# Performance work log

Hardware: AMD Instinct MI355X
Metric: run time of the kernel (lower is better)

Reference implementation:

```python
import jax, jax.numpy as jnp
import numpy as np

NUM_EMBEDDINGS = 1024
EMBEDDING_DIM = 256
COMMITMENT_COST = 0.25
N_TOKENS = 65536


def setup_inputs() -> dict:
    key = jax.random.key(0)
    k1, k2 = jax.random.split(key)
    z = jax.random.normal(k1, (N_TOKENS, EMBEDDING_DIM), dtype=jnp.float32)
    # codebook init as in the module: uniform in [-1/K, 1/K]
    embedding = jax.random.uniform(
        k2, (NUM_EMBEDDINGS, EMBEDDING_DIM),
        minval=-1.0 / NUM_EMBEDDINGS, maxval=1.0 / NUM_EMBEDDINGS,
        dtype=jnp.float32)
    return {"z": z, "embedding": embedding}


def reference(z, embedding):
    # squared euclidean distances: ||z||^2 + ||e||^2 - 2 z.e^T   -> [N, K]
    z_sq = jnp.sum(z ** 2, axis=1, keepdims=True)          # [N, 1]
    emb_sq = jnp.sum(embedding ** 2, axis=1)               # [K]
    dot = jnp.dot(z, embedding.T)                          # [N, K]
    distances = z_sq + emb_sq - 2.0 * dot
    indices = jnp.argmin(distances, axis=1)                # [N]
    z_q = embedding[indices]                               # [N, D] gather
    loss = (jnp.mean((jax.lax.stop_gradient(z) - z_q) ** 2)
            + COMMITMENT_COST * jnp.mean((jax.lax.stop_gradient(z_q) - z) ** 2))
    z_q_st = z + jax.lax.stop_gradient(z_q - z)            # straight-through
    return (z_q_st, loss, indices)
```

## Files before the change

kernel.cpp:

```cpp
#include <hip/hip_runtime.h>
#include <hip/hip_bf16.h>

#define NTOK   65536
#define KCODES 1024
#define DIM    256
#define LOSS_OFF ((size_t)NTOK * DIM)
#define IDX_OFF  (LOSS_OFF + 1)

#define MARGA 2e-4f

#define SC_ZSQ    0
#define SC_A1     65536
#define SC_LOSS2  131072
#define SC_ESQ    196608
#define SC_ESQNH  197632
#define SC_PART   198656
#define SC_WCNT   198720
#define SC_WCNT2  198721
#define SC_CNTG   198784
#define SC_LISTS  264320
#define SC_WLIST  788608
#define SC_WLIST2 854144
#define SC_EHIMG  858240
#define SC_ZIMG   989312
#define SC_PAIRD  9377920

typedef __attribute__((ext_vector_type(8))) short short8;
typedef __attribute__((ext_vector_type(4))) float f32x4;

__device__ __forceinline__ unsigned f2bf(float x) {
    unsigned u = __float_as_uint(x);
    return (u + 0x7FFFu + ((u >> 16) & 1u)) >> 16;
}

__device__ __forceinline__ void gload16(const void* g, void* l) {
    __builtin_amdgcn_global_load_lds((const __attribute__((address_space(1))) unsigned int*)g,
                                     (__attribute__((address_space(3))) unsigned int*)l,
                                     16, 0, 0);
}

__device__ __forceinline__ float faithful_d(const float* __restrict__ z,
                                            const float* __restrict__ emb,
                                            float zsq, float esq, int tok, int c) {
    const float4* zr = (const float4*)(z + (size_t)tok * DIM);
    const float4* er = (const float4*)(emb + (size_t)c * DIM);
    float acc = 0.f;
#pragma unroll 8
    for (int q = 0; q < 64; ++q) {
        float4 a = zr[q], b = er[q];
        acc = fmaf(a.x, b.x, acc); acc = fmaf(a.y, b.y, acc);
        acc = fmaf(a.z, b.z, acc); acc = fmaf(a.w, b.w, acc);
    }
    float t1 = zsq + esq;
    return t1 - 2.0f * acc;
}

__device__ __forceinline__ float np_rowsq256_wave(const float* row, int sub) {
    const int j = sub & 7, half = sub >> 3;
    const float* a = row + half * 128 + j;
    float r = 0.f;
#pragma unroll
    for (int i = 0; i < 16; ++i) {
        float v = a[i * 8];
        float sq = v * v;
        asm volatile("" : "+v"(sq));
        r += sq;
    }
    float t = r + __shfl_xor(r, 1, 64);
    t = t + __shfl_xor(t, 2, 64);
    t = t + __shfl_xor(t, 4, 64);
    t = t + __shfl_xor(t, 8, 64);
    return t;
}

__global__ __launch_bounds__(256) void vq_prep_esq(const float* __restrict__ emb,
                                                   float* __restrict__ esq,
                                                   float* __restrict__ esqnh,
                                                   int* __restrict__ wcnt,
                                                   int* __restrict__ wcnt2) {
    if (blockIdx.x == 0 && threadIdx.x == 0) { *wcnt = 0; *wcnt2 = 0; }
    int code = blockIdx.x * 16 + (threadIdx.x >> 4);
    int sub = threadIdx.x & 15;
    float tot = np_rowsq256_wave(emb + (size_t)code * DIM, sub);
    if (sub == 0) { esq[code] = tot; esqnh[code] = -0.5f * tot; }
}

__global__ __launch_bounds__(256) void vq_prep_z(const float* __restrict__ z,
                                                 float* __restrict__ zsq,
                                                 unsigned short* __restrict__ zimg) {
    int tok = blockIdx.x * 16 + (threadIdx.x >> 4);
    int sub = threadIdx.x & 15;
    float tot = np_rowsq256_wave(z + (size_t)tok * DIM, sub);
    if (sub == 0) zsq[tok] = tot;

    const float* src = z + (size_t)tok * DIM + sub * 16;
    float4 v0 = *(const float4*)&src[0],  v1 = *(const float4*)&src[4];
    float4 v2 = *(const float4*)&src[8],  v3 = *(const float4*)&src[12];
    uint4 p0, p1;
    p0.x = f2bf(v0.x) | (f2bf(v0.y) << 16);  p0.y = f2bf(v0.z) | (f2bf(v0.w) << 16);
    p0.z = f2bf(v1.x) | (f2bf(v1.y) << 16);  p0.w = f2bf(v1.z) | (f2bf(v1.w) << 16);
    p1.x = f2bf(v2.x) | (f2bf(v2.y) << 16);  p1.y = f2bf(v2.z) | (f2bf(v2.w) << 16);
    p1.z = f2bf(v3.x) | (f2bf(v3.y) << 16);  p1.w = f2bf(v3.z) | (f2bf(v3.w) << 16);

    int bid = tok >> 6, tf = (tok >> 4) & 3, sl = tok & 15;
    int g0 = sub * 2, g1 = g0 + 1;
    size_t rowbase = ((size_t)bid * 4 + tf) * 8;
    char* d0 = (char*)zimg + ((rowbase + (g0 >> 2)) << 10) + (((g0 & 3) * 16 + sl) << 4);
    char* d1 = (char*)zimg + ((rowbase + (g1 >> 2)) << 10) + (((g1 & 3) * 16 + sl) << 4);
    *(uint4*)d0 = p0;
    *(uint4*)d1 = p1;
}

__global__ __launch_bounds__(256) void vq_prep_eimg(const float* __restrict__ emb,
                                                    unsigned short* __restrict__ img) {
    int job = blockIdx.x * 256 + threadIdx.x;
    int code = job >> 3, ks = job & 7;
    int cc = (code >> 6) & 3, lcl = (code >> 8) * 64 + (code & 63);
    const float* src = emb + (size_t)code * DIM + ks * 32;
    char* base = (char*)img + (size_t)(cc * 8 + ks) * 16384;
#pragma unroll
    for (int q = 0; q < 4; ++q) {
        float4 v0 = *(const float4*)&src[q * 8];
        float4 v1 = *(const float4*)&src[q * 8 + 4];
        uint4 p;
        p.x = f2bf(v0.x) | (f2bf(v0.y) << 16);
        p.y = f2bf(v0.z) | (f2bf(v0.w) << 16);
        p.z = f2bf(v1.x) | (f2bf(v1.y) << 16);
        p.w = f2bf(v1.z) | (f2bf(v1.w) << 16);
        *(uint4*)(base + lcl * 64 + ((q * 16) ^ (((lcl >> 1) & 3) << 4))) = p;
    }
}

template<int PASS>
__global__ __launch_bounds__(256, 2) void vq_gemm(const unsigned short* __restrict__ zimg,
                                                  const unsigned short* __restrict__ img,
                                                  const float* __restrict__ esqnh,
                                                  const float* __restrict__ zsq,
                                                  float* __restrict__ a1,
                                                  int* __restrict__ wcnt,
                                                  int* __restrict__ wlist,
                                                  int* __restrict__ cntg,
                                                  int* __restrict__ listsg,
                                                  float* __restrict__ loss2,
                                                  float* __restrict__ dout) {
    __shared__ __align__(16) short eh_s[2][8192];
    __shared__ float a1w_s[4][64];
    __shared__ int cnt_s[64];
    __shared__ int lists_s[512];

    const int tid = threadIdx.x, bid = blockIdx.x;
    const int w = tid >> 6, l = tid & 63;
    const int t0 = bid * 64;

    short8 zf[4][8];
#pragma unroll
    for (int tf = 0; tf < 4; ++tf)
#pragma unroll
        for (int ks = 0; ks < 8; ++ks)
            zf[tf][ks] = *(const short8*)((const char*)zimg +
                           ((((size_t)bid * 4 + tf) * 8 + ks) << 10) + (size_t)l * 16);

    if (PASS == 2 && tid < 64) cnt_s[tid] = 0;
    {
        const char* gs = (const char*)img + w * 4096 + (size_t)l * 16;
        char* ld = (char*)&eh_s[0][0] + w * 4096;
#pragma unroll
        for (int i = 0; i < 4; ++i) gload16(gs + i * 1024, ld + i * 1024);
    }
    __syncthreads();

    float thrv[4], amax[4];
#pragma unroll
    for (int tf = 0; tf < 4; ++tf) {
        amax[tf] = -3.4e38f;
        if (PASS == 2) thrv[tf] = a1[t0 + tf * 16 + (l & 15)] - MARGA;
    }

    f32x4 acc[4][4];

#pragma unroll
    for (int c = 0; c < 4; ++c) {
#pragma unroll
        for (int f = 0; f < 4; ++f) {
            f32x4 e4 = *(const f32x4*)&esqnh[w * 256 + c * 64 + f * 16 + (l >> 4) * 4];
#pragma unroll
            for (int tf = 0; tf < 4; ++tf) acc[f][tf] = e4;
        }
#pragma unroll
        for (int ks = 0; ks < 8; ++ks) {
            int s = c * 8 + ks, buf = s & 1;
            if (s < 31) {
                const char* gs = (const char*)img + (size_t)(s + 1) * 16384 + w * 4096 + (size_t)l * 16;
                char* ld = (char*)&eh_s[buf ^ 1][0] + w * 4096;
#pragma unroll
                for (int i = 0; i < 4; ++i) gload16(gs + i * 1024, ld + i * 1024);
            }
            short8 afr[4];
#pragma unroll
            for (int f = 0; f < 4; ++f) {
                int lcl = w * 64 + f * 16 + (l & 15);
                int byte = lcl * 64 + (((l >> 4) * 16) ^ (((lcl >> 1) & 3) << 4));
                afr[f] = *(const short8*)((const char*)&eh_s[buf][0] + byte);
            }
#pragma unroll
            for (int f = 0; f < 4; ++f)
#pragma unroll
                for (int tf = 0; tf < 4; ++tf)
                    acc[f][tf] = __builtin_amdgcn_mfma_f32_16x16x32_bf16(
                        afr[f], zf[tf][ks], acc[f][tf], 0, 0, 0);
            __syncthreads();
        }
        if (PASS == 1) {
#pragma unroll
            for (int tf = 0; tf < 4; ++tf) {
                float m0 = fmaxf(fmaxf(acc[0][tf][0], acc[0][tf][1]), fmaxf(acc[0][tf][2], acc[0][tf][3]));
                float m1 = fmaxf(fmaxf(acc[1][tf][0], acc[1][tf][1]), fmaxf(acc[1][tf][2], acc[1][tf][3]));
                float m2 = fmaxf(fmaxf(acc[2][tf][0], acc[2][tf][1]), fmaxf(acc[2][tf][2], acc[2][tf][3]));
                float m3 = fmaxf(fmaxf(acc[3][tf][0], acc[3][tf][1]), fmaxf(acc[3][tf][2], acc[3][tf][3]));
                amax[tf] = fmaxf(amax[tf], fmaxf(fmaxf(m0, m1), fmaxf(m2, m3)));
            }
        } else {
#pragma unroll
            for (int tf = 0; tf < 4; ++tf) {
                int tokl = tf * 16 + (l & 15);
#pragma unroll
                for (int f = 0; f < 4; ++f)
#pragma unroll
                    for (int r = 0; r < 4; ++r) {
                        float a = acc[f][tf][r];
                        if (a >= thrv[tf]) {
                            int code = w * 256 + c * 64 + f * 16 + (l >> 4) * 4 + r;
                            int pos = atomicAdd(&cnt_s[tokl], 1);
                            if (pos < 8) lists_s[tokl * 8 + pos] = code;
                        }
                    }
            }
        }
    }

    if (PASS == 1) {
#pragma unroll
        for (int tf = 0; tf < 4; ++tf) {
            float m = amax[tf];
            m = fmaxf(m, __shfl_xor(m, 16, 64));
            m = fmaxf(m, __shfl_xor(m, 32, 64));
            if (l < 16) a1w_s[w][tf * 16 + l] = m;
        }
        __syncthreads();
        if (tid < 64)
            a1[t0 + tid] = fmaxf(fmaxf(a1w_s[0][tid], a1w_s[1][tid]),
                                 fmaxf(a1w_s[2][tid], a1w_s[3][tid]));
    } else {
        __syncthreads();
        if (tid < 64) {
            int t = t0 + tid, ct = cnt_s[tid];
            if (ct == 1) {
                dout[IDX_OFF + t] = (float)lists_s[tid * 8];
                loss2[t] = fmaf(-2.f, a1[t], zsq[t]);
            } else {
                int pos = atomicAdd(wcnt, 1);
                wlist[pos] = t;
                cntg[t] = ct;
                int m = ct < 8 ? ct : 8;
                for (int i = 0; i < m; ++i) listsg[t * 8 + i] = lists_s[tid * 8 + i];
            }
        }
    }
}

__global__ __launch_bounds__(256) void vq_pairs(const float* __restrict__ z,
                                                const float* __restrict__ emb,
                                                const float* __restrict__ zsq,
                                                const float* __restrict__ esq,
                                                const int* __restrict__ wcnt,
                                                const int* __restrict__ wlist,
                                                const int* __restrict__ cntg,
                                                const int* __restrict__ listsg,
                                                int* __restrict__ wcnt2,
                                                int* __restrict__ wlist2,
                                                float* __restrict__ paird) {
    const int n = wcnt[0];
    const int total = 8 * n;
    for (int p = blockIdx.x * 256 + threadIdx.x; p < total; p += 2048 * 256) {
        int q = p >> 3, slot = p & 7;
        int tok = wlist[q];
        int ct = cntg[tok];
        if (ct == 0 || ct > 8) {
            if (slot == 0) {
                int pos = atomicAdd(wcnt2, 1);
                if (pos < 4096) wlist2[pos] = tok;
            }
            continue;
        }
        if (slot >= ct) continue;
        int code = listsg[tok * 8 + slot];
        paird[p] = faithful_d(z, emb, zsq[tok], esq[code], tok, code);
    }
}

__global__ __launch_bounds__(256) void vq_pick(const float* __restrict__ paird,
                                               const int* __restrict__ wcnt,
                                               const int* __restrict__ wlist,
                                               const int* __restrict__ cntg,
                                               const int* __restrict__ listsg,
                                               float* __restrict__ loss2,
                                               float* __restrict__ dout) {
    const int n = wcnt[0];
    for (int q = blockIdx.x * 256 + threadIdx.x; q < n; q += 256 * 256) {
        int tok = wlist[q];
        int ct = cntg[tok];
        if (ct == 0 || ct > 8) continue;
        float db = paird[q * 8];
        int cb = listsg[tok * 8];
        for (int i = 1; i < ct; ++i) {
            float d = paird[q * 8 + i];
            int c = listsg[tok * 8 + i];
            if (d < db || (d == db && c < cb)) { db = d; cb = c; }
        }
        dout[IDX_OFF + tok] = (float)cb;
        loss2[tok] = db;
    }
}

__global__ __launch_bounds__(256) void vq_decide_scan(const float* __restrict__ z,
                                                      const float* __restrict__ emb,
                                                      const float* __restrict__ zsq,
                                                      const float* __restrict__ esq,
                                                      const int* __restrict__ wcnt2,
                                                      const int* __restrict__ wlist2,
                                                      float* __restrict__ loss2,
                                                      float* __restrict__ dout) {
    __shared__ __align__(16) float zrow[DIM];
    __shared__ float dred[256];
    __shared__ int   ired[256];
    int n = wcnt2[0];
    if (n > 4096) n = 4096;
    const int tid = threadIdx.x;
    for (int job = blockIdx.x; job < n; job += 128) {
        int tok = wlist2[job];
        __syncthreads();
        if (tid < 64) ((float4*)zrow)[tid] = ((const float4*)(z + (size_t)tok * DIM))[tid];
        __syncthreads();
        float zq = zsq[tok];
        float a0 = 0.f, a1v = 0.f, a2 = 0.f, a3 = 0.f;
        const float4* e0 = (const float4*)(emb + (size_t)(tid      ) * DIM);
        const float4* e1 = (const float4*)(emb + (size_t)(tid + 256) * DIM);
        const float4* e2 = (const float4*)(emb + (size_t)(tid + 512) * DIM);
        const float4* e3 = (const float4*)(emb + (size_t)(tid + 768) * DIM);
#pragma unroll
        for (int seg = 0; seg < 4; ++seg) {
#pragma unroll
            for (int qq = 0; qq < 16; ++qq) {
                float4 a = ((float4*)zrow)[seg * 16 + qq];
                float4 b0 = e0[seg * 16 + qq], b1 = e1[seg * 16 + qq];
                float4 b2 = e2[seg * 16 + qq], b3 = e3[seg * 16 + qq];
                a0 = fmaf(a.x, b0.x, a0); a0 = fmaf(a.y, b0.y, a0);
                a0 = fmaf(a.z, b0.z, a0); a0 = fmaf(a.w, b0.w, a0);
                a1v = fmaf(a.x, b1.x, a1v); a1v = fmaf(a.y, b1.y, a1v);
                a1v = fmaf(a.z, b1.z, a1v); a1v = fmaf(a.w, b1.w, a1v);
                a2 = fmaf(a.x, b2.x, a2); a2 = fmaf(a.y, b2.y, a2);
                a2 = fmaf(a.z, b2.z, a2); a2 = fmaf(a.w, b2.w, a2);
                a3 = fmaf(a.x, b3.x, a3); a3 = fmaf(a.y, b3.y, a3);
                a3 = fmaf(a.z, b3.z, a3); a3 = fmaf(a.w, b3.w, a3);
            }
        }
        float d0 = (zq + esq[tid      ]) - 2.0f * a0;
        float d1 = (zq + esq[tid + 256]) - 2.0f * a1v;
        float d2 = (zq + esq[tid + 512]) - 2.0f * a2;
        float d3 = (zq + esq[tid + 768]) - 2.0f * a3;
        float db = d0; int cb = tid;
        if (d1 < db) { db = d1; cb = tid + 256; }
        if (d2 < db) { db = d2; cb = tid + 512; }
        if (d3 < db) { db = d3; cb = tid + 768; }
        dred[tid] = db; ired[tid] = cb;
        __syncthreads();
        for (int step = 128; step >= 1; step >>= 1) {
            if (tid < step) {
                float od = dred[tid + step]; int oi = ired[tid + step];
                if (od < dred[tid] || (od == dred[tid] && oi < ired[tid])) {
                    dred[tid] = od; ired[tid] = oi;
                }
            }
            __syncthreads();
        }
        if (tid == 0) {
            dout[IDX_OFF + tok] = (float)ired[0];
            loss2[tok] = dred[0];
        }
    }
}

__global__ __launch_bounds__(256) void vq_sum(const float* __restrict__ loss2,
                                              float* __restrict__ part) {
    __shared__ float ws[4];
    float s = 0.f;
#pragma unroll
    for (int q = 0; q < 4; ++q)
        s += loss2[blockIdx.x * 1024 + q * 256 + threadIdx.x];
#pragma unroll
    for (int m = 1; m < 64; m <<= 1) s += __shfl_xor(s, m, 64);
    if ((threadIdx.x & 63) == 0) ws[threadIdx.x >> 6] = s;
    __syncthreads();
    if (threadIdx.x == 0) part[blockIdx.x] = ws[0] + ws[1] + ws[2] + ws[3];
}

__global__ __launch_bounds__(64) void vq_final(const float* __restrict__ part,
                                               float* __restrict__ dout) {
    double s = (double)part[threadIdx.x];
#pragma unroll
    for (int m = 1; m < 64; m <<= 1) s += __shfl_xor(s, m, 64);
    if (threadIdx.x == 0) dout[LOSS_OFF] = (float)(s * 1.25 / 16777216.0);
}

__global__ __launch_bounds__(256) void vq_gather(const float* __restrict__ emb,
                                                 float* __restrict__ dout) {
    const int w = threadIdx.x >> 6, l = threadIdx.x & 63;
    for (int tok = blockIdx.x * 4 + w; tok < NTOK; tok += 2048 * 4) {
        int widx = (int)dout[IDX_OFF + tok];
        float4 ev = *(const float4*)&emb[(size_t)widx * DIM + l * 4];
        *(float4*)&dout[(size_t)tok * DIM + l * 4] = ev;
    }
}

extern "C" void kernel_launch(void* const* d_in, const int* in_sizes, int n_in,
                              void* d_out, int out_size, void* d_ws, size_t ws_size,
                              hipStream_t stream) {
    const float* z   = (const float*)d_in[0];
    const float* emb = (const float*)d_in[1];
    float* out = (float*)d_out;

    float* zsq   = out + SC_ZSQ;
    float* a1    = out + SC_A1;
    float* loss2 = out + SC_LOSS2;
    float* esq   = out + SC_ESQ;
    float* esqnh = out + SC_ESQNH;
    float* part  = out + SC_PART;
    int*   wcnt  = (int*)(out + SC_WCNT);
    int*   wcnt2 = (int*)(out + SC_WCNT2);
    int*   cntg  = (int*)(out + SC_CNTG);
    int*   listsg= (int*)(out + SC_LISTS);
    int*   wlist = (int*)(out + SC_WLIST);
    int*   wlist2= (int*)(out + SC_WLIST2);
    float* paird = out + SC_PAIRD;
    unsigned short* img  = (unsigned short*)(out + SC_EHIMG);
    unsigned short* zimg = (unsigned short*)(out + SC_ZIMG);

    vq_prep_esq <<<64,   256, 0, stream>>>(emb, esq, esqnh, wcnt, wcnt2);
    vq_prep_z   <<<4096, 256, 0, stream>>>(z, zsq, zimg);
    vq_prep_eimg<<<32,   256, 0, stream>>>(emb, img);
    vq_gemm<1>  <<<1024, 256, 0, stream>>>(zimg, img, esqnh, zsq, a1, wcnt, wlist, cntg, listsg, loss2, out);
    vq_gemm<2>  <<<1024, 256, 0, stream>>>(zimg, img, esqnh, zsq, a1, wcnt, wlist, cntg, listsg, loss2, out);
    vq_pairs    <<<2048, 256, 0, stream>>>(z, emb, zsq, esq, wcnt, wlist, cntg, listsg, wcnt2, wlist2, paird);
    vq_pick     <<<256,  256, 0, stream>>>(paird, wcnt, wlist, cntg, listsg, loss2, out);
    vq_decide_scan<<<128, 256, 0, stream>>>(z, emb, zsq, esq, wcnt2, wlist2, loss2, out);
    vq_sum      <<<64,   256, 0, stream>>>(loss2, part);
    vq_final    <<<1,    64,  0, stream>>>(part, out);
    vq_gather   <<<2048, 256, 0, stream>>>(emb, out);
}
```

Before: 160.1 us.

## Fuse two-pass GEMM argmin into a single pass with running-max candidate filtering

The separate max pass and candidate-collection pass of the bf16 MFMA distance GEMM are merged into one kernel. Each chunk tracks a running per-token max, records candidates above the running threshold together with their scores in shared memory, then re-filters them against the final max. This halves the GEMM work and the reads of z and the codebook. In exchange, early chunks can admit more candidates, which risks overflowing the 16-slot buffer and pushing more tokens to the slow fallback path.

```diff
diff --git a/kernel.cpp b/kernel.cpp
--- a/kernel.cpp
+++ b/kernel.cpp
@@ -10,7 +10,6 @@
 #define MARGA 2e-4f
 
 #define SC_ZSQ    0
-#define SC_A1     65536
 #define SC_LOSS2  131072
 #define SC_ESQ    196608
 #define SC_ESQNH  197632
@@ -131,12 +130,10 @@
     }
 }
 
-template<int PASS>
 __global__ __launch_bounds__(256, 2) void vq_gemm(const unsigned short* __restrict__ zimg,
                                                   const unsigned short* __restrict__ img,
                                                   const float* __restrict__ esqnh,
                                                   const float* __restrict__ zsq,
-                                                  float* __restrict__ a1,
                                                   int* __restrict__ wcnt,
                                                   int* __restrict__ wlist,
                                                   int* __restrict__ cntg,
@@ -145,8 +142,9 @@
                                                   float* __restrict__ dout) {
     __shared__ __align__(16) short eh_s[2][8192];
     __shared__ float a1w_s[4][64];
-    __shared__ int cnt_s[64];
-    __shared__ int lists_s[512];
+    __shared__ int   cnt_s[64];
+    __shared__ int   lists_s[64 * 16];
+    __shared__ float avals_s[64 * 16];
 
     const int tid = threadIdx.x, bid = blockIdx.x;
     const int w = tid >> 6, l = tid & 63;
@@ -160,7 +158,7 @@
             zf[tf][ks] = *(const short8*)((const char*)zimg +
                            ((((size_t)bid * 4 + tf) * 8 + ks) << 10) + (size_t)l * 16);
 
-    if (PASS == 2 && tid < 64) cnt_s[tid] = 0;
+    if (tid < 64) cnt_s[tid] = 0;
     {
         const char* gs = (const char*)img + w * 4096 + (size_t)l * 16;
         char* ld = (char*)&eh_s[0][0] + w * 4096;
@@ -169,13 +167,7 @@
     }
     __syncthreads();
 
-    float thrv[4], amax[4];
-#pragma unroll
-    for (int tf = 0; tf < 4; ++tf) {
-        amax[tf] = -3.4e38f;
-        if (PASS == 2) thrv[tf] = a1[t0 + tf * 16 + (l & 15)] - MARGA;
-    }
-
+    float m_run[4] = {-3.4e38f, -3.4e38f, -3.4e38f, -3.4e38f};
     f32x4 acc[4][4];
 
 #pragma unroll
@@ -210,59 +202,68 @@
                         afr[f], zf[tf][ks], acc[f][tf], 0, 0, 0);
             __syncthreads();
         }
-        if (PASS == 1) {
-#pragma unroll
-            for (int tf = 0; tf < 4; ++tf) {
-                float m0 = fmaxf(fmaxf(acc[0][tf][0], acc[0][tf][1]), fmaxf(acc[0][tf][2], acc[0][tf][3]));
-                float m1 = fmaxf(fmaxf(acc[1][tf][0], acc[1][tf][1]), fmaxf(acc[1][tf][2], acc[1][tf][3]));
-                float m2 = fmaxf(fmaxf(acc[2][tf][0], acc[2][tf][1]), fmaxf(acc[2][tf][2], acc[2][tf][3]));
-                float m3 = fmaxf(fmaxf(acc[3][tf][0], acc[3][tf][1]), fmaxf(acc[3][tf][2], acc[3][tf][3]));
-                amax[tf] = fmaxf(amax[tf], fmaxf(fmaxf(m0, m1), fmaxf(m2, m3)));
-            }
-        } else {
-#pragma unroll
-            for (int tf = 0; tf < 4; ++tf) {
-                int tokl = tf * 16 + (l & 15);
-#pragma unroll
-                for (int f = 0; f < 4; ++f)
-#pragma unroll
-                    for (int r = 0; r < 4; ++r) {
-                        float a = acc[f][tf][r];
-                        if (a >= thrv[tf]) {
-                            int code = w * 256 + c * 64 + f * 16 + (l >> 4) * 4 + r;
-                            int pos = atomicAdd(&cnt_s[tokl], 1);
-                            if (pos < 8) lists_s[tokl * 8 + pos] = code;
+#pragma unroll
+        for (int tf = 0; tf < 4; ++tf) {
+            float m0 = fmaxf(fmaxf(acc[0][tf][0], acc[0][tf][1]), fmaxf(acc[0][tf][2], acc[0][tf][3]));
+            float m1 = fmaxf(fmaxf(acc[1][tf][0], acc[1][tf][1]), fmaxf(acc[1][tf][2], acc[1][tf][3]));
+            float m2 = fmaxf(fmaxf(acc[2][tf][0], acc[2][tf][1]), fmaxf(acc[2][tf][2], acc[2][tf][3]));
+            float m3 = fmaxf(fmaxf(acc[3][tf][0], acc[3][tf][1]), fmaxf(acc[3][tf][2], acc[3][tf][3]));
+            float tm = fmaxf(fmaxf(m0, m1), fmaxf(m2, m3));
+            tm = fmaxf(tm, __shfl_xor(tm, 16, 64));
+            tm = fmaxf(tm, __shfl_xor(tm, 32, 64));
+            m_run[tf] = fmaxf(m_run[tf], tm);
+            float thr = m_run[tf] - MARGA;
+            int tokl = tf * 16 + (l & 15);
+#pragma unroll
+            for (int f = 0; f < 4; ++f)
+#pragma unroll
+                for (int r = 0; r < 4; ++r) {
+                    float a = acc[f][tf][r];
+                    if (a >= thr) {
+                        int code = w * 256 + c * 64 + f * 16 + (l >> 4) * 4 + r;
+                        int pos = atomicAdd(&cnt_s[tokl], 1);
+                        if (pos < 16) {
+                            lists_s[tokl * 16 + pos] = code;
+                            avals_s[tokl * 16 + pos] = a;
                         }
                     }
-            }
-        }
-    }
-
-    if (PASS == 1) {
-#pragma unroll
-        for (int tf = 0; tf < 4; ++tf) {
-            float m = amax[tf];
-            m = fmaxf(m, __shfl_xor(m, 16, 64));
-            m = fmaxf(m, __shfl_xor(m, 32, 64));
-            if (l < 16) a1w_s[w][tf * 16 + l] = m;
-        }
-        __syncthreads();
-        if (tid < 64)
-            a1[t0 + tid] = fmaxf(fmaxf(a1w_s[0][tid], a1w_s[1][tid]),
-                                 fmaxf(a1w_s[2][tid], a1w_s[3][tid]));
-    } else {
-        __syncthreads();
-        if (tid < 64) {
-            int t = t0 + tid, ct = cnt_s[tid];
-            if (ct == 1) {
-                dout[IDX_OFF + t] = (float)lists_s[tid * 8];
-                loss2[t] = fmaf(-2.f, a1[t], zsq[t]);
+                }
+        }
+    }
+
+#pragma unroll
+    for (int tf = 0; tf < 4; ++tf)
+        if (l < 16) a1w_s[w][tf * 16 + l] = m_run[tf];
+    __syncthreads();
+
+    if (tid < 64) {
+        int t = t0 + tid;
+        float a1v = fmaxf(fmaxf(a1w_s[0][tid], a1w_s[1][tid]),
+                          fmaxf(a1w_s[2][tid], a1w_s[3][tid]));
+        int ct_raw = cnt_s[tid];
+        if (ct_raw > 16) {
+            int pos = atomicAdd(wcnt, 1);
+            wlist[pos] = t;
+            cntg[t] = 999;
+        } else {
+            float thr = a1v - MARGA;
+            int kept = 0, first = 0;
+            for (int i = 0; i < ct_raw; ++i) {
+                float av = avals_s[tid * 16 + i];
+                if (av >= thr) {
+                    int code = lists_s[tid * 16 + i];
+                    if (kept == 0) first = code;
+                    if (kept < 8) listsg[(size_t)t * 8 + kept] = code;
+                    ++kept;
+                }
+            }
+            if (kept == 1) {
+                dout[IDX_OFF + t] = (float)first;
+                loss2[t] = fmaf(-2.f, a1v, zsq[t]);
             } else {
                 int pos = atomicAdd(wcnt, 1);
                 wlist[pos] = t;
-                cntg[t] = ct;
-                int m = ct < 8 ? ct : 8;
-                for (int i = 0; i < m; ++i) listsg[t * 8 + i] = lists_s[tid * 8 + i];
+                cntg[t] = (kept > 8) ? 999 : kept;
             }
         }
     }
@@ -293,7 +294,7 @@
             continue;
         }
         if (slot >= ct) continue;
-        int code = listsg[tok * 8 + slot];
+        int code = listsg[(size_t)tok * 8 + slot];
         paird[p] = faithful_d(z, emb, zsq[tok], esq[code], tok, code);
     }
 }
@@ -311,10 +312,10 @@
         int ct = cntg[tok];
         if (ct == 0 || ct > 8) continue;
         float db = paird[q * 8];
-        int cb = listsg[tok * 8];
+        int cb = listsg[(size_t)tok * 8];
         for (int i = 1; i < ct; ++i) {
             float d = paird[q * 8 + i];
-            int c = listsg[tok * 8 + i];
+            int c = listsg[(size_t)tok * 8 + i];
             if (d < db || (d == db && c < cb)) { db = d; cb = c; }
         }
         dout[IDX_OFF + tok] = (float)cb;
@@ -430,7 +431,6 @@
     float* out = (float*)d_out;
 
     float* zsq   = out + SC_ZSQ;
-    float* a1    = out + SC_A1;
     float* loss2 = out + SC_LOSS2;
     float* esq   = out + SC_ESQ;
     float* esqnh = out + SC_ESQNH;
@@ -448,8 +448,7 @@
     vq_prep_esq <<<64,   256, 0, stream>>>(emb, esq, esqnh, wcnt, wcnt2);
     vq_prep_z   <<<4096, 256, 0, stream>>>(z, zsq, zimg);
     vq_prep_eimg<<<32,   256, 0, stream>>>(emb, img);
-    vq_gemm<1>  <<<1024, 256, 0, stream>>>(zimg, img, esqnh, zsq, a1, wcnt, wlist, cntg, listsg, loss2, out);
-    vq_gemm<2>  <<<1024, 256, 0, stream>>>(zimg, img, esqnh, zsq, a1, wcnt, wlist, cntg, listsg, loss2, out);
+    vq_gemm     <<<1024, 256, 0, stream>>>(zimg, img, esqnh, zsq, wcnt, wlist, cntg, listsg, loss2, out);
     vq_pairs    <<<2048, 256, 0, stream>>>(z, emb, zsq, esq, wcnt, wlist, cntg, listsg, wcnt2, wlist2, paird);
     vq_pick     <<<256,  256, 0, stream>>>(paird, wcnt, wlist, cntg, listsg, loss2, out);
     vq_decide_scan<<<128, 256, 0, stream>>>(z, emb, zsq, esq, wcnt2, wlist2, loss2, out);
```

Result: slower. 233.6 us (+45.9%).
